# Kernel tuning notes

Measured on AMD Instinct MI355X. Metric: run time of the kernel, lower is better.

The kernel has to match this reference:

```python
import jax, jax.numpy as jnp
import numpy as np

EMBED_DIM = 1024
NUM_HEADS = 16
HEAD_DIM = EMBED_DIM // NUM_HEADS


def setup_inputs() -> dict:
    key = jax.random.key(0)
    ks = jax.random.split(key, 6)
    s = 1.0 / np.sqrt(EMBED_DIM)
    return {
        "x": jax.random.normal(ks[0], (4, 2048, EMBED_DIM), dtype=jnp.float32),
        "Wq": jax.random.uniform(ks[1], (EMBED_DIM, EMBED_DIM), jnp.float32, -s, s),
        "Wk": jax.random.uniform(ks[2], (EMBED_DIM, EMBED_DIM), jnp.float32, -s, s),
        "Wv": jax.random.uniform(ks[3], (EMBED_DIM, EMBED_DIM), jnp.float32, -s, s),
        "Wo": jax.random.uniform(ks[4], (EMBED_DIM, EMBED_DIM), jnp.float32, -s, s),
        "bo": jax.random.uniform(ks[5], (EMBED_DIM,), jnp.float32, -s, s),
    }


def reference(x, Wq, Wk, Wv, Wo, bo):
    B, S, E = x.shape
    H, D = NUM_HEADS, HEAD_DIM
    # torch Linear: x @ W.T ; reshape to [B, H, S, D]
    q = (x @ Wq.T).reshape(B, S, H, D).transpose(0, 2, 1, 3)
    k = (x @ Wk.T).reshape(B, S, H, D).transpose(0, 2, 1, 3)
    v = (x @ Wv.T).reshape(B, S, H, D).transpose(0, 2, 1, 3)
    scores = jnp.einsum("bhqd,bhkd->bhqk", q, k) / jnp.sqrt(jnp.float32(D))
    attn = jax.nn.softmax(scores, axis=-1)  # dropout is identity in eval mode
    out = jnp.einsum("bhqk,bhkd->bhqd", attn, v)
    out = out.transpose(0, 2, 1, 3).reshape(B, S, E)
    return out @ Wo.T + bo
```

## Files before the change

kernel.cpp:

```cpp
#include <hip/hip_runtime.h>
#include <hip/hip_bf16.h>
#include <math.h>

#define B_ 4
#define S_ 2048
#define E_ 1024
#define H_ 16
#define D_ 64
#define M_ (B_*S_)
#define NKV 32

typedef __attribute__((ext_vector_type(8))) short short8;
typedef __attribute__((ext_vector_type(4))) short short4_t;
typedef __attribute__((ext_vector_type(4))) float f32x4;
typedef __attribute__((ext_vector_type(16))) float f32x16;

static __device__ __forceinline__ short f2bf(float f){
  union { float f; unsigned u; } v; v.f = f;
  unsigned u = v.u + 0x7FFFu + ((v.u >> 16) & 1u);
  return (short)(u >> 16);
}

__global__ void cast_all(const float* __restrict__ x,
    const float* __restrict__ wq, const float* __restrict__ wk,
    const float* __restrict__ wv, const float* __restrict__ wo,
    short8* __restrict__ xb, short8* __restrict__ wqb, short8* __restrict__ wkb,
    short8* __restrict__ wvb, short8* __restrict__ wob){
  int bid = blockIdx.x;
  const float* src; short8* dst; int i;
  if (bid < 4096) { src = x; dst = xb; i = bid*256 + threadIdx.x; }
  else {
    int k = (bid - 4096) >> 9;
    i = ((bid - 4096) & 511)*256 + threadIdx.x;
    src = k==0 ? wq : k==1 ? wk : k==2 ? wv : wo;
    dst = k==0 ? wqb : k==1 ? wkb : k==2 ? wvb : wob;
  }
  const float4* s4 = (const float4*)src;
  float4 a = s4[2*i], b = s4[2*i+1];
  short8 o;
  o[0]=f2bf(a.x); o[1]=f2bf(a.y); o[2]=f2bf(a.z); o[3]=f2bf(a.w);
  o[4]=f2bf(b.x); o[5]=f2bf(b.y); o[6]=f2bf(b.z); o[7]=f2bf(b.w);
  dst[i]=o;
}

#define GLOAD16(g, l) __builtin_amdgcn_global_load_lds( \
    (const __attribute__((address_space(1))) void*)(g), \
    (__attribute__((address_space(3))) void*)(l), 16, 0, 0)

__global__ __launch_bounds__(512,1) void gemm_qkv(const short* __restrict__ A,
      const short* __restrict__ Wf, short* __restrict__ Qo, short* __restrict__ Ko,
      short* __restrict__ Vto, float u)
{
  extern __shared__ char LDSc[];
  const int tid = threadIdx.x;
  const int w = tid >> 6, lane = tid & 63;
  const int l15 = lane & 15, l4 = lane >> 4;
  const int rx = l15 & 7;
  const int wm = w >> 2, wn = w & 3;
  const int m0 = blockIdx.x * 256;
  const int n0 = blockIdx.y * 192;

  const int lanerow = lane >> 3;
  const int lchunk8 = ((lane & 7) ^ lanerow) * 8;
  const short* Aq = A  + (size_t)(m0 + w*8 + lanerow)*1024 + lchunk8;
  const short* Bq = Wf + (size_t)(n0 + w*8 + lanerow)*1024 + lchunk8;

  #define STA(kt,i) GLOAD16(Aq + (size_t)((i)*64)*1024 + (kt)*64, \
      LDSc + ((kt)&1)*57344 + (i)*8192 + w*1024);
  #define STB(kt,i) GLOAD16(Bq + (size_t)((i)*64)*1024 + (kt)*64, \
      LDSc + ((kt)&1)*57344 + 32768 + (i)*8192 + w*1024);

  #define BARF __builtin_amdgcn_s_barrier(); \
               asm volatile("" ::: "memory"); \
               __builtin_amdgcn_sched_barrier(0);

  f32x4 acc[8][3] = {};

  STA(0,0) STA(0,1) STA(0,2) STA(0,3)
  STB(0,0) STB(0,1) STB(0,2)
  asm volatile("s_waitcnt vmcnt(0)" ::: "memory");
  BARF

  #define RDA(QM) \
    _Pragma("unroll") for (int i_ = 0; i_ < 4; ++i_) \
    _Pragma("unroll") for (int ks_ = 0; ks_ < 2; ++ks_) \
      af_[i_][ks_] = *(const short8*)(Ab + (wm*128 + (QM)*64 + i_*16 + l15)*128 + (((ks_*4 + l4) ^ rx)*16));
  #define RDB \
    _Pragma("unroll") for (int j_ = 0; j_ < 3; ++j_) \
    _Pragma("unroll") for (int ks_ = 0; ks_ < 2; ++ks_) \
      bf_[j_][ks_] = *(const short8*)(Bb + (wn*48 + j_*16 + l15)*128 + (((ks_*4 + l4) ^ rx)*16));
  #define MF(QM) \
    __builtin_amdgcn_s_setprio(1); \
    _Pragma("unroll") for (int i_ = 0; i_ < 4; ++i_) \
    _Pragma("unroll") for (int j_ = 0; j_ < 3; ++j_) \
    _Pragma("unroll") for (int ks_ = 0; ks_ < 2; ++ks_) \
      acc[(QM)*4+i_][j_] = __builtin_amdgcn_mfma_f32_16x16x32_bf16( \
          af_[i_][ks_], bf_[j_][ks_], acc[(QM)*4+i_][j_], 0,0,0); \
    __builtin_amdgcn_s_setprio(0);

  for (int k = 0; k < 16; ++k) {
    const char* Ab = LDSc + (k & 1)*57344;
    const char* Bb = Ab + 32768;
    const bool st = (k < 15);
    short8 af_[4][2], bf_[3][2];
    RDA(0)
    RDB
    if (st) { STA(k+1,0) STA(k+1,1) STA(k+1,2) STA(k+1,3) }
    BARF
    MF(0)
    BARF
    RDA(1)
    if (st) { STB(k+1,0) STB(k+1,1) STB(k+1,2) }
    BARF
    MF(1)
    asm volatile("s_waitcnt vmcnt(0)" ::: "memory");
    BARF
  }
  #undef RDA
  #undef RDB
  #undef MF
  #undef STA
  #undef STB
  #undef BARF

  #pragma unroll
  for (int i = 0; i < 8; ++i) {
    int row = m0 + wm*128 + i*16 + 4*l4;
    int b = row >> 11;
    int s0 = row & 2047;
    #pragma unroll
    for (int j = 0; j < 3; ++j) {
      int col = n0 + wn*48 + j*16 + l15;
      int sel = col >> 10;
      int colm = col & 1023;
      int h = colm >> 6, d = colm & 63;
      if (sel == 2) {
        short4_t pk;
        pk[0]=f2bf(acc[i][j][0]); pk[1]=f2bf(acc[i][j][1]);
        pk[2]=f2bf(acc[i][j][2]); pk[3]=f2bf(acc[i][j][3]);
        *(short4_t*)(Vto + (((size_t)(b*H_ + h))*D_ + d)*S_ + s0) = pk;
      } else {
        short* O = sel ? Ko : Qo;
        float sc = sel ? 1.0f : u;
        #pragma unroll
        for (int r = 0; r < 4; ++r) {
          int s = (s0 + r) & 2047;
          O[(((size_t)(b*H_ + h))*S_ + s)*D_ + d] = f2bf(acc[i][j][r]*sc);
        }
      }
    }
  }
}

__global__ __launch_bounds__(256,2) void gemm_out(const short* __restrict__ A,
      const short* __restrict__ W, float* __restrict__ out,
      const float* __restrict__ bias)
{
  __shared__ short AL[128*32];
  __shared__ short BL[128*32];
  const int tid = threadIdx.x;
  const int w = tid >> 6, lane = tid & 63;
  const int l15 = lane & 15, l4 = lane >> 4;
  const int m0 = blockIdx.x * 128;
  const int n0 = blockIdx.y * 128;
  const int wr = w >> 1, wc = w & 1;
  f32x4 acc[4][4] = {};

  const short* ga = A + (size_t)(m0 + (tid>>2))*1024 + (tid&3)*8;
  const short* gb = W + (size_t)(n0 + (tid>>2))*1024 + (tid&3)*8;

  for (int kt = 0; kt < 32; ++kt) {
    const int ko = kt*32;
    #pragma unroll
    for (int p = 0; p < 2; ++p) {
      GLOAD16(ga + (size_t)(p*64)*1024 + ko, (char*)AL + p*4096 + w*1024);
      GLOAD16(gb + (size_t)(p*64)*1024 + ko, (char*)BL + p*4096 + w*1024);
    }
    __syncthreads();
    short8 af[4], bw[4];
    #pragma unroll
    for (int i = 0; i < 4; ++i) {
      af[i] = *(const short8*)(AL + (wr*64 + i*16 + l15)*32 + 8*l4);
      bw[i] = *(const short8*)(BL + (wc*64 + i*16 + l15)*32 + 8*l4);
    }
    #pragma unroll
    for (int i = 0; i < 4; ++i)
      #pragma unroll
      for (int j = 0; j < 4; ++j)
        acc[i][j] = __builtin_amdgcn_mfma_f32_16x16x32_bf16(af[i], bw[j], acc[i][j], 0,0,0);
    __syncthreads();
  }

  #pragma unroll
  for (int i = 0; i < 4; ++i) {
    int row = m0 + wr*64 + i*16 + 4*l4;
    #pragma unroll
    for (int j = 0; j < 4; ++j) {
      int col = n0 + wc*64 + j*16 + l15;
      float bz = bias[col];
      #pragma unroll
      for (int r = 0; r < 4; ++r)
        out[(size_t)(row + r)*1024 + col] = acc[i][j][r] + bz;
    }
  }
}

static __device__ __forceinline__ unsigned cvtpk(float lo, float hi){
  unsigned d; asm("v_cvt_pk_bf16_f32 %0, %1, %2" : "=v"(d) : "v"(lo), "v"(hi)); return d;
}
static __device__ __forceinline__ void plswap(unsigned &a, unsigned &b){
  asm("v_permlane32_swap_b32 %0, %1" : "+v"(a), "+v"(b));
}
template<int BASE>
static __device__ __forceinline__ short8 pfrag(const f32x16 &s){
  unsigned w01 = cvtpk(s[BASE+0], s[BASE+1]);
  unsigned w23 = cvtpk(s[BASE+2], s[BASE+3]);
  unsigned w45 = cvtpk(s[BASE+4], s[BASE+5]);
  unsigned w67 = cvtpk(s[BASE+6], s[BASE+7]);
  plswap(w01, w45);
  plswap(w23, w67);
  union { unsigned u[4]; short8 s8; } r;
  r.u[0]=w01; r.u[1]=w23; r.u[2]=w45; r.u[3]=w67;
  return r.s8;
}

__global__ __launch_bounds__(256,4) void attn_kernel(const short* __restrict__ Qb,
    const short* __restrict__ Kb, const short* __restrict__ Vtb, short* __restrict__ Ob)
{
  __shared__ short KL[2][64*64];
  __shared__ short VL[2][64*64];
  const int tid = threadIdx.x, w = tid >> 6, lane = tid & 63;
  const int l31 = lane & 31, hi = lane >> 5;
  const int rx7 = l31 & 7;

  const int linear = blockIdx.x;
  const int swz = (linear & 7)*128 + (linear >> 3);
  const int bh = swz >> 4;
  const int b = bh >> 4, h = bh & 15;
  const int q0 = (swz & 15) * 128;

  const short* Qg = Qb + ((size_t)bh*S_ + q0)*D_;
  const short* Kg = Kb + (size_t)bh*S_*D_;
  const short* Vg = Vtb + (size_t)bh*D_*S_;

  const int srow = tid >> 3;
  const int scol = ((tid & 7) ^ (srow & 7)) * 8;

  #define STAGE(t, bi) { \
    GLOAD16(Kg + (size_t)((t)*64 +      srow)*D_ + scol, (char*)KL[bi] + w*1024); \
    GLOAD16(Kg + (size_t)((t)*64 + 32 + srow)*D_ + scol, (char*)KL[bi] + 4096 + w*1024); \
    GLOAD16(Vg + (size_t)(     srow)*S_ + (t)*64 + scol, (char*)VL[bi] + w*1024); \
    GLOAD16(Vg + (size_t)(32 + srow)*S_ + (t)*64 + scol, (char*)VL[bi] + 4096 + w*1024); }

  STAGE(0, 0)

  const int qrow = w*32 + l31;
  short8 qf[4];
  #pragma unroll
  for (int t = 0; t < 4; ++t)
    qf[t] = *(const short8*)(Qg + (size_t)qrow*D_ + (2*t + hi)*8);

  f32x16 oacc[2] = {};
  float l_run = 0.f;

  for (int kv = 0; kv < NKV; ++kv) {
    const int cur = kv & 1;
    if (kv < NKV-1) {
      STAGE(kv+1, cur^1)
      asm volatile("s_waitcnt vmcnt(4)" ::: "memory");
    } else {
      asm volatile("s_waitcnt vmcnt(0)" ::: "memory");
    }
    __builtin_amdgcn_s_barrier();
    asm volatile("" ::: "memory");
    __builtin_amdgcn_sched_barrier(0);

    f32x16 st[2] = {};
    __builtin_amdgcn_s_setprio(1);
    #pragma unroll
    for (int t = 0; t < 4; ++t) {
      int co = ((2*t + hi) ^ rx7)*16;
      short8 ka0 = *(const short8*)((char*)KL[cur] + l31*128 + co);
      short8 ka1 = *(const short8*)((char*)KL[cur] + (32 + l31)*128 + co);
      st[0] = __builtin_amdgcn_mfma_f32_32x32x16_bf16(ka0, qf[t], st[0], 0,0,0);
      st[1] = __builtin_amdgcn_mfma_f32_32x32x16_bf16(ka1, qf[t], st[1], 0,0,0);
    }
    __builtin_amdgcn_s_setprio(0);

    #pragma unroll
    for (int r = 0; r < 16; ++r) st[0][r] = __builtin_amdgcn_exp2f(st[0][r]);
    #pragma unroll
    for (int r = 0; r < 16; ++r) st[1][r] = __builtin_amdgcn_exp2f(st[1][r]);
    {
      f32x16 sv = st[0] + st[1];
      float sa = (sv[0]+sv[1]) + (sv[2]+sv[3]);
      float sb = (sv[4]+sv[5]) + (sv[6]+sv[7]);
      float sc = (sv[8]+sv[9]) + (sv[10]+sv[11]);
      float sd = (sv[12]+sv[13]) + (sv[14]+sv[15]);
      l_run += (sa+sb) + (sc+sd);
    }

    short8 pf[4];
    pf[0] = pfrag<0>(st[0]);
    pf[1] = pfrag<8>(st[0]);
    pf[2] = pfrag<0>(st[1]);
    pf[3] = pfrag<8>(st[1]);

    __builtin_amdgcn_s_setprio(1);
    #pragma unroll
    for (int t = 0; t < 4; ++t) {
      int co = ((2*t + hi) ^ rx7)*16;
      short8 va0 = *(const short8*)((char*)VL[cur] + l31*128 + co);
      short8 va1 = *(const short8*)((char*)VL[cur] + (32 + l31)*128 + co);
      oacc[0] = __builtin_amdgcn_mfma_f32_32x32x16_bf16(va0, pf[t], oacc[0], 0,0,0);
      oacc[1] = __builtin_amdgcn_mfma_f32_32x32x16_bf16(va1, pf[t], oacc[1], 0,0,0);
    }
    __builtin_amdgcn_s_setprio(0);
    __builtin_amdgcn_sched_barrier(0);
    asm volatile("" ::: "memory");
    __builtin_amdgcn_s_barrier();
    asm volatile("" ::: "memory");
  }
  #undef STAGE

  float lt = l_run + __shfl_xor(l_run, 32);
  float inv = 1.f / lt;
  int s = q0 + qrow;
  short* orow = Ob + ((size_t)(b*S_ + s))*E_ + h*64;
  #pragma unroll
  for (int r = 0; r < 16; r += 2) {
    int d0 = (r & 3) + 8*(r >> 2) + 4*hi;
    unsigned pa = (unsigned short)f2bf(oacc[0][r]*inv) |
                  ((unsigned)(unsigned short)f2bf(oacc[0][r+1]*inv) << 16);
    unsigned pb = (unsigned short)f2bf(oacc[1][r]*inv) |
                  ((unsigned)(unsigned short)f2bf(oacc[1][r+1]*inv) << 16);
    *(unsigned*)(orow + d0) = pa;
    *(unsigned*)(orow + 32 + d0) = pb;
  }
}

extern "C" void kernel_launch(void* const* d_in, const int* in_sizes, int n_in,
                              void* d_out, int out_size, void* d_ws, size_t ws_size,
                              hipStream_t stream) {
  const float* x  = (const float*)d_in[0];
  const float* Wq = (const float*)d_in[1];
  const float* Wk = (const float*)d_in[2];
  const float* Wv = (const float*)d_in[3];
  const float* Wo = (const float*)d_in[4];
  const float* bo = (const float*)d_in[5];

  char* ws = (char*)d_ws;
  short* xb  = (short*)(ws);
  short* Wqb = (short*)(ws + (16u<<20));
  short* Wkb = (short*)(ws + (18u<<20));
  short* Wvb = (short*)(ws + (20u<<20));
  short* Wob = (short*)(ws + (22u<<20));
  short* Qb  = (short*)(ws + (24u<<20));
  short* Kb  = (short*)(ws + (40u<<20));
  short* Vtb = (short*)(ws + (56u<<20));
  short* Ab  = (short*)(ws + (72u<<20));

  cast_all<<<4096 + 4*512, 256, 0, stream>>>(x, Wq, Wk, Wv, Wo,
      (short8*)xb, (short8*)Wqb, (short8*)Wkb, (short8*)Wvb, (short8*)Wob);

  const float u = 0.18033688011112042f;
  gemm_qkv<<<dim3(32, 16), 512, 114688, stream>>>(xb, Wqb, Qb, Kb, Vtb, u);

  attn_kernel<<<1024, 256, 0, stream>>>(Qb, Kb, Vtb, Ab);

  gemm_out<<<dim3(64, 8), 256, 0, stream>>>(Ab, Wob, (float*)d_out, bo);
}
```

Before: 178.2 us.

## Port pipelined 256x128 GEMM to output projection and compute softmax sum via MFMA

The output-projection GEMM is rebuilt on the same double-buffered, swizzled, 512-thread pipeline used by the QKV GEMM. It uses 256x128 tiles and 64-wide K steps instead of the simple 128x128 single-buffer loop with 32-wide K steps. Separately, the attention kernel drops the per-iteration scalar row-sum reduction and instead accumulates the softmax denominator with an extra MFMA against a vector of bf16 ones. This makes the sum use the same bf16-rounded probabilities as the PV product. The trade-off is one extra MFMA per PV step, a new accumulator register array, and larger LDS use for the output GEMM.

```diff
diff --git a/kernel.cpp b/kernel.cpp
--- a/kernel.cpp
+++ b/kernel.cpp
@@ -47,6 +47,10 @@
     (const __attribute__((address_space(1))) void*)(g), \
     (__attribute__((address_space(3))) void*)(l), 16, 0, 0)
 
+#define BARF __builtin_amdgcn_s_barrier(); \
+             asm volatile("" ::: "memory"); \
+             __builtin_amdgcn_sched_barrier(0);
+
 __global__ __launch_bounds__(512,1) void gemm_qkv(const short* __restrict__ A,
       const short* __restrict__ Wf, short* __restrict__ Qo, short* __restrict__ Ko,
       short* __restrict__ Vto, float u)
@@ -70,10 +74,6 @@
   #define STB(kt,i) GLOAD16(Bq + (size_t)((i)*64)*1024 + (kt)*64, \
       LDSc + ((kt)&1)*57344 + 32768 + (i)*8192 + w*1024);
 
-  #define BARF __builtin_amdgcn_s_barrier(); \
-               asm volatile("" ::: "memory"); \
-               __builtin_amdgcn_sched_barrier(0);
-
   f32x4 acc[8][3] = {};
 
   STA(0,0) STA(0,1) STA(0,2) STA(0,3)
@@ -121,7 +121,6 @@
   #undef MF
   #undef STA
   #undef STB
-  #undef BARF
 
   #pragma unroll
   for (int i = 0; i < 8; ++i) {
@@ -152,51 +151,83 @@
   }
 }
 
-__global__ __launch_bounds__(256,2) void gemm_out(const short* __restrict__ A,
+__global__ __launch_bounds__(512,1) void gemm_out(const short* __restrict__ A,
       const short* __restrict__ W, float* __restrict__ out,
       const float* __restrict__ bias)
 {
-  __shared__ short AL[128*32];
-  __shared__ short BL[128*32];
+  extern __shared__ char LDSc[];
   const int tid = threadIdx.x;
   const int w = tid >> 6, lane = tid & 63;
   const int l15 = lane & 15, l4 = lane >> 4;
-  const int m0 = blockIdx.x * 128;
+  const int rx = l15 & 7;
+  const int wm = w >> 2, wn = w & 3;
+  const int m0 = blockIdx.x * 256;
   const int n0 = blockIdx.y * 128;
-  const int wr = w >> 1, wc = w & 1;
-  f32x4 acc[4][4] = {};
-
-  const short* ga = A + (size_t)(m0 + (tid>>2))*1024 + (tid&3)*8;
-  const short* gb = W + (size_t)(n0 + (tid>>2))*1024 + (tid&3)*8;
-
-  for (int kt = 0; kt < 32; ++kt) {
-    const int ko = kt*32;
-    #pragma unroll
-    for (int p = 0; p < 2; ++p) {
-      GLOAD16(ga + (size_t)(p*64)*1024 + ko, (char*)AL + p*4096 + w*1024);
-      GLOAD16(gb + (size_t)(p*64)*1024 + ko, (char*)BL + p*4096 + w*1024);
-    }
-    __syncthreads();
-    short8 af[4], bw[4];
-    #pragma unroll
-    for (int i = 0; i < 4; ++i) {
-      af[i] = *(const short8*)(AL + (wr*64 + i*16 + l15)*32 + 8*l4);
-      bw[i] = *(const short8*)(BL + (wc*64 + i*16 + l15)*32 + 8*l4);
-    }
-    #pragma unroll
-    for (int i = 0; i < 4; ++i)
-      #pragma unroll
-      for (int j = 0; j < 4; ++j)
-        acc[i][j] = __builtin_amdgcn_mfma_f32_16x16x32_bf16(af[i], bw[j], acc[i][j], 0,0,0);
-    __syncthreads();
-  }
-
-  #pragma unroll
-  for (int i = 0; i < 4; ++i) {
-    int row = m0 + wr*64 + i*16 + 4*l4;
-    #pragma unroll
-    for (int j = 0; j < 4; ++j) {
-      int col = n0 + wc*64 + j*16 + l15;
+
+  const int lanerow = lane >> 3;
+  const int lchunk8 = ((lane & 7) ^ lanerow) * 8;
+  const short* Aq = A + (size_t)(m0 + w*8 + lanerow)*1024 + lchunk8;
+  const short* Bq = W + (size_t)(n0 + w*8 + lanerow)*1024 + lchunk8;
+
+  #define STA(kt,i) GLOAD16(Aq + (size_t)((i)*64)*1024 + (kt)*64, \
+      LDSc + ((kt)&1)*49152 + (i)*8192 + w*1024);
+  #define STB(kt,i) GLOAD16(Bq + (size_t)((i)*64)*1024 + (kt)*64, \
+      LDSc + ((kt)&1)*49152 + 32768 + (i)*8192 + w*1024);
+
+  f32x4 acc[8][2] = {};
+
+  STA(0,0) STA(0,1) STA(0,2) STA(0,3)
+  STB(0,0) STB(0,1)
+  asm volatile("s_waitcnt vmcnt(0)" ::: "memory");
+  BARF
+
+  #define RDA(QM) \
+    _Pragma("unroll") for (int i_ = 0; i_ < 4; ++i_) \
+    _Pragma("unroll") for (int ks_ = 0; ks_ < 2; ++ks_) \
+      af_[i_][ks_] = *(const short8*)(Ab + (wm*128 + (QM)*64 + i_*16 + l15)*128 + (((ks_*4 + l4) ^ rx)*16));
+  #define RDB \
+    _Pragma("unroll") for (int j_ = 0; j_ < 2; ++j_) \
+    _Pragma("unroll") for (int ks_ = 0; ks_ < 2; ++ks_) \
+      bf_[j_][ks_] = *(const short8*)(Bb + (wn*32 + j_*16 + l15)*128 + (((ks_*4 + l4) ^ rx)*16));
+  #define MF(QM) \
+    __builtin_amdgcn_s_setprio(1); \
+    _Pragma("unroll") for (int i_ = 0; i_ < 4; ++i_) \
+    _Pragma("unroll") for (int j_ = 0; j_ < 2; ++j_) \
+    _Pragma("unroll") for (int ks_ = 0; ks_ < 2; ++ks_) \
+      acc[(QM)*4+i_][j_] = __builtin_amdgcn_mfma_f32_16x16x32_bf16( \
+          af_[i_][ks_], bf_[j_][ks_], acc[(QM)*4+i_][j_], 0,0,0); \
+    __builtin_amdgcn_s_setprio(0);
+
+  for (int k = 0; k < 16; ++k) {
+    const char* Ab = LDSc + (k & 1)*49152;
+    const char* Bb = Ab + 32768;
+    const bool st = (k < 15);
+    short8 af_[4][2], bf_[2][2];
+    RDA(0)
+    RDB
+    if (st) { STA(k+1,0) STA(k+1,1) STA(k+1,2) STA(k+1,3) }
+    BARF
+    MF(0)
+    BARF
+    RDA(1)
+    if (st) { STB(k+1,0) STB(k+1,1) }
+    BARF
+    MF(1)
+    asm volatile("s_waitcnt vmcnt(0)" ::: "memory");
+    BARF
+  }
+  #undef RDA
+  #undef RDB
+  #undef MF
+  #undef STA
+  #undef STB
+
+  #pragma unroll
+  for (int i = 0; i < 8; ++i) {
+    int row = m0 + wm*128 + i*16 + 4*l4;
+    #pragma unroll
+    for (int j = 0; j < 2; ++j) {
+      int col = n0 + wn*32 + j*16 + l15;
       float bz = bias[col];
       #pragma unroll
       for (int r = 0; r < 4; ++r)
@@ -260,8 +291,12 @@
   for (int t = 0; t < 4; ++t)
     qf[t] = *(const short8*)(Qg + (size_t)qrow*D_ + (2*t + hi)*8);
 
+  short8 ones;
+  #pragma unroll
+  for (int t = 0; t < 8; ++t) ones[t] = (short)0x3F80;
+
   f32x16 oacc[2] = {};
-  float l_run = 0.f;
+  f32x16 lacc = {};
 
   for (int kv = 0; kv < NKV; ++kv) {
     const int cur = kv & 1;
@@ -291,14 +326,6 @@
     for (int r = 0; r < 16; ++r) st[0][r] = __builtin_amdgcn_exp2f(st[0][r]);
     #pragma unroll
     for (int r = 0; r < 16; ++r) st[1][r] = __builtin_amdgcn_exp2f(st[1][r]);
-    {
-      f32x16 sv = st[0] + st[1];
-      float sa = (sv[0]+sv[1]) + (sv[2]+sv[3]);
-      float sb = (sv[4]+sv[5]) + (sv[6]+sv[7]);
-      float sc = (sv[8]+sv[9]) + (sv[10]+sv[11]);
-      float sd = (sv[12]+sv[13]) + (sv[14]+sv[15]);
-      l_run += (sa+sb) + (sc+sd);
-    }
 
     short8 pf[4];
     pf[0] = pfrag<0>(st[0]);
@@ -314,6 +341,7 @@
       short8 va1 = *(const short8*)((char*)VL[cur] + (32 + l31)*128 + co);
       oacc[0] = __builtin_amdgcn_mfma_f32_32x32x16_bf16(va0, pf[t], oacc[0], 0,0,0);
       oacc[1] = __builtin_amdgcn_mfma_f32_32x32x16_bf16(va1, pf[t], oacc[1], 0,0,0);
+      lacc = __builtin_amdgcn_mfma_f32_32x32x16_bf16(ones, pf[t], lacc, 0,0,0);
     }
     __builtin_amdgcn_s_setprio(0);
     __builtin_amdgcn_sched_barrier(0);
@@ -323,8 +351,7 @@
   }
   #undef STAGE
 
-  float lt = l_run + __shfl_xor(l_run, 32);
-  float inv = 1.f / lt;
+  float inv = 1.f / lacc[0];
   int s = q0 + qrow;
   short* orow = Ob + ((size_t)(b*S_ + s))*E_ + h*64;
   #pragma unroll
@@ -368,5 +395,5 @@
 
   attn_kernel<<<1024, 256, 0, stream>>>(Qb, Kb, Vtb, Ab);
 
-  gemm_out<<<dim3(64, 8), 256, 0, stream>>>(Ab, Wob, (float*)d_out, bo);
-}
+  gemm_out<<<dim3(32, 8), 512, 98304, stream>>>(Ab, Wob, (float*)d_out, bo);
+}
```

After: 175.9 us (median of 3 runs). Within noise of the previous version (-1.2%).
